# Optimization experiments

Measured on AMD Instinct MI355X. Metric: run time of the kernel, lower is better.

## Reference

```python
import jax, jax.numpy as jnp
import numpy as np

REG_DIAG = 0.01   # per-position regularizer added inside the loop in the original
REG_EPS = 1e-05   # global regularizer added after the loop


def setup_inputs() -> dict:
    key = jax.random.key(0)
    B, C, HW = 32, 128, 3136
    embedding = jax.random.normal(key, (B, C, HW), dtype=jnp.float32)
    return {"embedding": embedding}


def reference(embedding):
    # embedding: (B, C, HW)
    B, C, HW = embedding.shape
    mean = jnp.mean(embedding, axis=0)                     # (C, HW)
    centered = embedding - mean[None, :, :]                # (B, C, HW)
    # Per-position sample covariance: cov[i] = X_m^T X_m / (B-1), X_m = (B, C) slice at position i.
    cov = jnp.einsum('bci,bdi->icd', centered, centered) / (B - 1)  # (HW, C, C)
    eye = jnp.eye(C, dtype=embedding.dtype)
    cov = cov + (REG_DIAG + REG_EPS) * eye[None, :, :]
    inv_covariance = jnp.linalg.inv(cov)                   # batched inverse, (HW, C, C)
    return (mean, inv_covariance)
```

## Files before the change

### kernel.cpp

```cpp
#include <hip/hip_runtime.h>

#define HW 3136
#define NB 32
#define NC 128
#define XST 132
#define SST 36
#define LAMV 0.01001f

static __device__ __forceinline__ float2 pka0(float2 c, float2 v, float2 a) {
  float2 d;
  asm("v_pk_fma_f32 %0, %1, %2, %3 op_sel:[0,0,0] op_sel_hi:[0,1,1]"
      : "=v"(d) : "v"(c), "v"(v), "v"(a));
  return d;
}
static __device__ __forceinline__ float2 pka1(float2 c, float2 v, float2 a) {
  float2 d;
  asm("v_pk_fma_f32 %0, %1, %2, %3 op_sel:[1,0,0] op_sel_hi:[1,1,1]"
      : "=v"(d) : "v"(c), "v"(v), "v"(a));
  return d;
}
static __device__ __forceinline__ float2 pke(float2 a, float2 b, float2 c) {
  float2 d;
  asm("v_pk_fma_f32 %0, %1, %2, %3"
      : "=v"(d) : "v"(a), "v"(b), "v"(c));
  return d;
}

__global__ __launch_bounds__(512, 8)
void mvg_kernel(const float* __restrict__ emb, float* __restrict__ out) {
  const int bid = blockIdx.x;
  const int pos = (bid & 7) * 392 + (bid >> 3);
  const int t = threadIdx.x;

  __shared__ __align__(16) float XcB[NB * XST];
  __shared__ __align__(16) float WB[NB * XST];
  __shared__ __align__(16) float SB[32 * SST];
  __shared__ float ms[NC];

  #pragma unroll
  for (int m = 0; m < 8; ++m) {
    const int idx = t + 512 * m;
    const int b = idx >> 7;
    const int c = idx & (NC - 1);
    XcB[b * XST + c] = emb[(size_t)b * (size_t)(NC * HW) + (size_t)c * HW + pos];
  }
  __syncthreads();

  if (t < NC) {
    float s = 0.f;
    #pragma unroll
    for (int b = 0; b < NB; ++b) s += XcB[b * XST + t];
    const float m = s * (1.0f / NB);
    ms[t] = m;
    out[(size_t)t * HW + pos] = m;
  }
  __syncthreads();

  #pragma unroll
  for (int m = 0; m < 8; ++m) {
    const int idx = t + 512 * m;
    const int b = idx >> 7;
    const int c = idx & (NC - 1);
    XcB[b * XST + c] -= ms[c];
  }
  __syncthreads();

  {
    const int i = t >> 4;
    const int j2 = t & 15;
    const float* xi = &XcB[i * XST];
    const float* xa = &XcB[(2 * j2) * XST];
    const float* xb = &XcB[(2 * j2 + 1) * XST];
    float2 accA = make_float2(0.f, 0.f), accB = make_float2(0.f, 0.f);
    #pragma unroll 8
    for (int c = 0; c < NC; c += 4) {
      const float4 vi = *(const float4*)&xi[c];
      const float4 va = *(const float4*)&xa[c];
      const float4 vb = *(const float4*)&xb[c];
      const float2 viL = make_float2(vi.x, vi.y), viH = make_float2(vi.z, vi.w);
      accA = pke(viL, make_float2(va.x, va.y), accA);
      accA = pke(viH, make_float2(va.z, va.w), accA);
      accB = pke(viL, make_float2(vb.x, vb.y), accB);
      accB = pke(viH, make_float2(vb.z, vb.w), accB);
    }
    const float s31 = 1.0f / 31.0f;
    SB[i * SST + 2 * j2]     = (accA.x + accA.y) * s31 + ((i == 2 * j2)     ? LAMV : 0.f);
    SB[i * SST + 2 * j2 + 1] = (accB.x + accB.y) * s31 + ((i == 2 * j2 + 1) ? LAMV : 0.f);
  }
  __syncthreads();

  if (t < 64) {
    const int r = t & 31;
    const int hb = (t >> 5) << 4;
    float m[16];
    #pragma unroll
    for (int j = 0; j < 4; ++j) {
      const float4 v = *(const float4*)&SB[r * SST + hb + 4 * j];
      m[4 * j] = v.x; m[4 * j + 1] = v.y; m[4 * j + 2] = v.z; m[4 * j + 3] = v.w;
    }

    #define SWEEP_K(K) {                                                    \
      float pc = m[(K) & 15] - ((r == (K)) ? 1.0f : 0.0f);                  \
      const float dm1 = __shfl(pc, (((K) >> 4) << 5) + (K), 64);            \
      const float cr  = __shfl(pc, (((K) >> 4) << 5) + r, 64);              \
      const float g = cr * __builtin_amdgcn_rcpf(dm1 + 1.0f);               \
      float hj[16];                                                         \
      _Pragma("unroll")                                                     \
      for (int j = 0; j < 16; ++j)                                          \
        hj[j] = __shfl(pc, (((K) >> 4) << 5) + hb + j, 64);                 \
      _Pragma("unroll")                                                     \
      for (int j = 0; j < 16; ++j) m[j] = fmaf(-g, hj[j], m[j]);            \
    }

    SWEEP_K(0)  SWEEP_K(1)  SWEEP_K(2)  SWEEP_K(3)
    SWEEP_K(4)  SWEEP_K(5)  SWEEP_K(6)  SWEEP_K(7)
    SWEEP_K(8)  SWEEP_K(9)  SWEEP_K(10) SWEEP_K(11)
    SWEEP_K(12) SWEEP_K(13) SWEEP_K(14) SWEEP_K(15)
    SWEEP_K(16) SWEEP_K(17) SWEEP_K(18) SWEEP_K(19)
    SWEEP_K(20) SWEEP_K(21) SWEEP_K(22) SWEEP_K(23)
    SWEEP_K(24) SWEEP_K(25) SWEEP_K(26) SWEEP_K(27)
    SWEEP_K(28) SWEEP_K(29) SWEEP_K(30) SWEEP_K(31)

    #pragma unroll
    for (int j = 0; j < 16; ++j) {
      const int col = hb + j;
      SB[r * SST + col] = (col == r) ? (2.0f - m[j]) : (-m[j]);
    }
  }
  __syncthreads();

  {
    const int s = t >> 4;
    const int C0 = (t & 15) << 3;
    float2 w01 = make_float2(0.f, 0.f), w23 = make_float2(0.f, 0.f);
    float2 w45 = make_float2(0.f, 0.f), w67 = make_float2(0.f, 0.f);
    #pragma unroll 2
    for (int j = 0; j < 32; j += 4) {
      const float4 sv = *(const float4*)&SB[s * SST + j];
      const float2 svL = make_float2(sv.x, sv.y);
      const float2 svH = make_float2(sv.z, sv.w);
      {
        const float* xr = &XcB[(j + 0) * XST + C0];
        const float4 a = *(const float4*)xr;
        const float4 b = *(const float4*)(xr + 4);
        w01 = pka0(svL, make_float2(a.x, a.y), w01);
        w23 = pka0(svL, make_float2(a.z, a.w), w23);
        w45 = pka0(svL, make_float2(b.x, b.y), w45);
        w67 = pka0(svL, make_float2(b.z, b.w), w67);
      }
      {
        const float* xr = &XcB[(j + 1) * XST + C0];
        const float4 a = *(const float4*)xr;
        const float4 b = *(const float4*)(xr + 4);
        w01 = pka1(svL, make_float2(a.x, a.y), w01);
        w23 = pka1(svL, make_float2(a.z, a.w), w23);
        w45 = pka1(svL, make_float2(b.x, b.y), w45);
        w67 = pka1(svL, make_float2(b.z, b.w), w67);
      }
      {
        const float* xr = &XcB[(j + 2) * XST + C0];
        const float4 a = *(const float4*)xr;
        const float4 b = *(const float4*)(xr + 4);
        w01 = pka0(svH, make_float2(a.x, a.y), w01);
        w23 = pka0(svH, make_float2(a.z, a.w), w23);
        w45 = pka0(svH, make_float2(b.x, b.y), w45);
        w67 = pka0(svH, make_float2(b.z, b.w), w67);
      }
      {
        const float* xr = &XcB[(j + 3) * XST + C0];
        const float4 a = *(const float4*)xr;
        const float4 b = *(const float4*)(xr + 4);
        w01 = pka1(svH, make_float2(a.x, a.y), w01);
        w23 = pka1(svH, make_float2(a.z, a.w), w23);
        w45 = pka1(svH, make_float2(b.x, b.y), w45);
        w67 = pka1(svH, make_float2(b.z, b.w), w67);
      }
    }
    *(float4*)&WB[s * XST + C0]     = make_float4(w01.x, w01.y, w23.x, w23.y);
    *(float4*)&WB[s * XST + C0 + 4] = make_float4(w45.x, w45.y, w67.x, w67.y);
  }
  __syncthreads();

  {
    const int rm = t >> 5;
    const int cm = t & 31;
    const int i0 = rm << 3;
    const int c0 = cm << 2;
    float2 aP[8][2];
    #pragma unroll
    for (int r = 0; r < 8; ++r) {
      aP[r][0] = make_float2(0.f, 0.f);
      aP[r][1] = make_float2(0.f, 0.f);
    }
    #pragma unroll 4
    for (int s = 0; s < 32; ++s) {
      const float4 cv0 = *(const float4*)&XcB[s * XST + i0];
      const float4 cv1 = *(const float4*)&XcB[s * XST + i0 + 4];
      const float4 rv  = *(const float4*)&WB[s * XST + c0];
      const float2 rL = make_float2(rv.x, rv.y), rH = make_float2(rv.z, rv.w);
      const float2 c01 = make_float2(cv0.x, cv0.y), c23 = make_float2(cv0.z, cv0.w);
      const float2 c45 = make_float2(cv1.x, cv1.y), c67 = make_float2(cv1.z, cv1.w);
      aP[0][0] = pka0(c01, rL, aP[0][0]); aP[0][1] = pka0(c01, rH, aP[0][1]);
      aP[1][0] = pka1(c01, rL, aP[1][0]); aP[1][1] = pka1(c01, rH, aP[1][1]);
      aP[2][0] = pka0(c23, rL, aP[2][0]); aP[2][1] = pka0(c23, rH, aP[2][1]);
      aP[3][0] = pka1(c23, rL, aP[3][0]); aP[3][1] = pka1(c23, rH, aP[3][1]);
      aP[4][0] = pka0(c45, rL, aP[4][0]); aP[4][1] = pka0(c45, rH, aP[4][1]);
      aP[5][0] = pka1(c45, rL, aP[5][0]); aP[5][1] = pka1(c45, rH, aP[5][1]);
      aP[6][0] = pka0(c67, rL, aP[6][0]); aP[6][1] = pka0(c67, rH, aP[6][1]);
      aP[7][0] = pka1(c67, rL, aP[7][0]); aP[7][1] = pka1(c67, rH, aP[7][1]);
    }
    const float ILAM = 1.0f / LAMV;
    const float IL31 = ILAM / 31.0f;
    float* o = out + (size_t)NC * HW + (size_t)pos * (NC * NC);
    #pragma unroll
    for (int r = 0; r < 8; ++r) {
      const int gr = i0 + r;
      float4 w;
      w.x = fmaf(-IL31, aP[r][0].x, (gr == c0 + 0) ? ILAM : 0.f);
      w.y = fmaf(-IL31, aP[r][0].y, (gr == c0 + 1) ? ILAM : 0.f);
      w.z = fmaf(-IL31, aP[r][1].x, (gr == c0 + 2) ? ILAM : 0.f);
      w.w = fmaf(-IL31, aP[r][1].y, (gr == c0 + 3) ? ILAM : 0.f);
      *(float4*)&o[(size_t)gr * NC + c0] = w;
    }
  }
}

extern "C" void kernel_launch(void* const* d_in, const int* in_sizes, int n_in,
                              void* d_out, int out_size, void* d_ws, size_t ws_size,
                              hipStream_t stream) {
  const float* emb = (const float*)d_in[0];
  float* out = (float*)d_out;
  mvg_kernel<<<HW, 512, 0, stream>>>(emb, out);
}
```

Measured before the change: 155.5 us.

## Exploit symmetry of inverse covariance and permute batch rows for Gram tiling

The final 128x128 inverse is symmetric, so only the upper-triangular 8x8 block tiles (136 blocks split across 272 threads) are computed, and each off-diagonal tile is written twice, once transposed. Batch rows are stored in permuted order (even/odd split) in shared memory so the 32x32 Gram step can use 16x16 threads, each producing a 2x2 register tile with more reuse. The W = S*Xc step likewise gives each thread two output rows. The intent is to roughly halve the FMA work in the last GEMM and cut LDS traffic. The cost is more idle threads, strided transposed global stores that coalesce less well, and extra index maths including a sqrt.

Result: faster. 145.8 us (-6.3%).

```diff
diff --git a/kernel.cpp b/kernel.cpp
--- a/kernel.cpp
+++ b/kernel.cpp
@@ -6,6 +6,7 @@
 #define XST 132
 #define SST 36
 #define LAMV 0.01001f
+#define SIG(r) (((((r) & 1)) << 4) | ((r) >> 1))
 
 static __device__ __forceinline__ float2 pka0(float2 c, float2 v, float2 a) {
   float2 d;
@@ -42,7 +43,7 @@
     const int idx = t + 512 * m;
     const int b = idx >> 7;
     const int c = idx & (NC - 1);
-    XcB[b * XST + c] = emb[(size_t)b * (size_t)(NC * HW) + (size_t)c * HW + pos];
+    XcB[SIG(b) * XST + c] = emb[(size_t)b * (size_t)(NC * HW) + (size_t)c * HW + pos];
   }
   __syncthreads();
 
@@ -65,37 +66,50 @@
   }
   __syncthreads();
 
-  {
-    const int i = t >> 4;
-    const int j2 = t & 15;
-    const float* xi = &XcB[i * XST];
-    const float* xa = &XcB[(2 * j2) * XST];
-    const float* xb = &XcB[(2 * j2 + 1) * XST];
-    float2 accA = make_float2(0.f, 0.f), accB = make_float2(0.f, 0.f);
+  if (t < 256) {
+    const int I = t >> 4;
+    const int J = t & 15;
+    const float* xi0 = &XcB[I * XST];
+    const float* xi1 = &XcB[(16 + I) * XST];
+    const float* xj0 = &XcB[J * XST];
+    const float* xj1 = &XcB[(16 + J) * XST];
+    float2 d00 = make_float2(0.f, 0.f), d01 = make_float2(0.f, 0.f);
+    float2 d10 = make_float2(0.f, 0.f), d11 = make_float2(0.f, 0.f);
     #pragma unroll 8
     for (int c = 0; c < NC; c += 4) {
-      const float4 vi = *(const float4*)&xi[c];
-      const float4 va = *(const float4*)&xa[c];
-      const float4 vb = *(const float4*)&xb[c];
-      const float2 viL = make_float2(vi.x, vi.y), viH = make_float2(vi.z, vi.w);
-      accA = pke(viL, make_float2(va.x, va.y), accA);
-      accA = pke(viH, make_float2(va.z, va.w), accA);
-      accB = pke(viL, make_float2(vb.x, vb.y), accB);
-      accB = pke(viH, make_float2(vb.z, vb.w), accB);
+      const float4 a0 = *(const float4*)&xi0[c];
+      const float4 a1 = *(const float4*)&xi1[c];
+      const float4 b0 = *(const float4*)&xj0[c];
+      const float4 b1 = *(const float4*)&xj1[c];
+      const float2 a0L = make_float2(a0.x, a0.y), a0H = make_float2(a0.z, a0.w);
+      const float2 a1L = make_float2(a1.x, a1.y), a1H = make_float2(a1.z, a1.w);
+      const float2 b0L = make_float2(b0.x, b0.y), b0H = make_float2(b0.z, b0.w);
+      const float2 b1L = make_float2(b1.x, b1.y), b1H = make_float2(b1.z, b1.w);
+      d00 = pke(a0L, b0L, d00); d00 = pke(a0H, b0H, d00);
+      d01 = pke(a0L, b1L, d01); d01 = pke(a0H, b1H, d01);
+      d10 = pke(a1L, b0L, d10); d10 = pke(a1H, b0H, d10);
+      d11 = pke(a1L, b1L, d11); d11 = pke(a1H, b1H, d11);
     }
     const float s31 = 1.0f / 31.0f;
-    SB[i * SST + 2 * j2]     = (accA.x + accA.y) * s31 + ((i == 2 * j2)     ? LAMV : 0.f);
-    SB[i * SST + 2 * j2 + 1] = (accB.x + accB.y) * s31 + ((i == 2 * j2 + 1) ? LAMV : 0.f);
+    const float dg = (I == J) ? LAMV : 0.f;
+    float2 e0, e1;
+    e0.x = (d00.x + d00.y) * s31 + dg;
+    e0.y = (d01.x + d01.y) * s31;
+    e1.x = (d10.x + d10.y) * s31;
+    e1.y = (d11.x + d11.y) * s31 + dg;
+    *(float2*)&SB[I * SST + 2 * J] = e0;
+    *(float2*)&SB[(16 + I) * SST + 2 * J] = e1;
   }
   __syncthreads();
 
   if (t < 64) {
     const int r = t & 31;
     const int hb = (t >> 5) << 4;
+    const int rs = SIG(r);
     float m[16];
     #pragma unroll
     for (int j = 0; j < 4; ++j) {
-      const float4 v = *(const float4*)&SB[r * SST + hb + 4 * j];
+      const float4 v = *(const float4*)&SB[rs * SST + hb + 4 * j];
       m[4 * j] = v.x; m[4 * j + 1] = v.y; m[4 * j + 2] = v.z; m[4 * j + 3] = v.w;
     }
 
@@ -124,68 +138,96 @@
     #pragma unroll
     for (int j = 0; j < 16; ++j) {
       const int col = hb + j;
-      SB[r * SST + col] = (col == r) ? (2.0f - m[j]) : (-m[j]);
-    }
-  }
-  __syncthreads();
-
-  {
-    const int s = t >> 4;
+      SB[rs * SST + col] = (col == r) ? (2.0f - m[j]) : (-m[j]);
+    }
+  }
+  __syncthreads();
+
+  if (t < 256) {
+    const int s2 = t >> 4;
     const int C0 = (t & 15) << 3;
-    float2 w01 = make_float2(0.f, 0.f), w23 = make_float2(0.f, 0.f);
-    float2 w45 = make_float2(0.f, 0.f), w67 = make_float2(0.f, 0.f);
+    float2 w0[4], w1[4];
+    #pragma unroll
+    for (int q = 0; q < 4; ++q) {
+      w0[q] = make_float2(0.f, 0.f);
+      w1[q] = make_float2(0.f, 0.f);
+    }
     #pragma unroll 2
     for (int j = 0; j < 32; j += 4) {
-      const float4 sv = *(const float4*)&SB[s * SST + j];
-      const float2 svL = make_float2(sv.x, sv.y);
-      const float2 svH = make_float2(sv.z, sv.w);
-      {
-        const float* xr = &XcB[(j + 0) * XST + C0];
-        const float4 a = *(const float4*)xr;
-        const float4 b = *(const float4*)(xr + 4);
-        w01 = pka0(svL, make_float2(a.x, a.y), w01);
-        w23 = pka0(svL, make_float2(a.z, a.w), w23);
-        w45 = pka0(svL, make_float2(b.x, b.y), w45);
-        w67 = pka0(svL, make_float2(b.z, b.w), w67);
-      }
-      {
-        const float* xr = &XcB[(j + 1) * XST + C0];
-        const float4 a = *(const float4*)xr;
-        const float4 b = *(const float4*)(xr + 4);
-        w01 = pka1(svL, make_float2(a.x, a.y), w01);
-        w23 = pka1(svL, make_float2(a.z, a.w), w23);
-        w45 = pka1(svL, make_float2(b.x, b.y), w45);
-        w67 = pka1(svL, make_float2(b.z, b.w), w67);
-      }
-      {
-        const float* xr = &XcB[(j + 2) * XST + C0];
-        const float4 a = *(const float4*)xr;
-        const float4 b = *(const float4*)(xr + 4);
-        w01 = pka0(svH, make_float2(a.x, a.y), w01);
-        w23 = pka0(svH, make_float2(a.z, a.w), w23);
-        w45 = pka0(svH, make_float2(b.x, b.y), w45);
-        w67 = pka0(svH, make_float2(b.z, b.w), w67);
-      }
-      {
-        const float* xr = &XcB[(j + 3) * XST + C0];
-        const float4 a = *(const float4*)xr;
-        const float4 b = *(const float4*)(xr + 4);
-        w01 = pka1(svH, make_float2(a.x, a.y), w01);
-        w23 = pka1(svH, make_float2(a.z, a.w), w23);
-        w45 = pka1(svH, make_float2(b.x, b.y), w45);
-        w67 = pka1(svH, make_float2(b.z, b.w), w67);
-      }
-    }
-    *(float4*)&WB[s * XST + C0]     = make_float4(w01.x, w01.y, w23.x, w23.y);
-    *(float4*)&WB[s * XST + C0 + 4] = make_float4(w45.x, w45.y, w67.x, w67.y);
-  }
-  __syncthreads();
-
-  {
-    const int rm = t >> 5;
-    const int cm = t & 31;
-    const int i0 = rm << 3;
-    const int c0 = cm << 2;
+      const float4 sv0 = *(const float4*)&SB[s2 * SST + j];
+      const float4 sv1 = *(const float4*)&SB[(16 + s2) * SST + j];
+      const float2 s0L = make_float2(sv0.x, sv0.y), s0H = make_float2(sv0.z, sv0.w);
+      const float2 s1L = make_float2(sv1.x, sv1.y), s1H = make_float2(sv1.z, sv1.w);
+      const int jh = j >> 1;
+      const float* xr0 = &XcB[jh * XST + C0];
+      const float* xr1 = &XcB[(16 + jh) * XST + C0];
+      const float* xr2 = &XcB[(jh + 1) * XST + C0];
+      const float* xr3 = &XcB[(16 + jh + 1) * XST + C0];
+      {
+        const float4 a = *(const float4*)xr0;
+        const float4 b = *(const float4*)(xr0 + 4);
+        w0[0] = pka0(s0L, make_float2(a.x, a.y), w0[0]);
+        w0[1] = pka0(s0L, make_float2(a.z, a.w), w0[1]);
+        w0[2] = pka0(s0L, make_float2(b.x, b.y), w0[2]);
+        w0[3] = pka0(s0L, make_float2(b.z, b.w), w0[3]);
+        w1[0] = pka0(s1L, make_float2(a.x, a.y), w1[0]);
+        w1[1] = pka0(s1L, make_float2(a.z, a.w), w1[1]);
+        w1[2] = pka0(s1L, make_float2(b.x, b.y), w1[2]);
+        w1[3] = pka0(s1L, make_float2(b.z, b.w), w1[3]);
+      }
+      {
+        const float4 a = *(const float4*)xr1;
+        const float4 b = *(const float4*)(xr1 + 4);
+        w0[0] = pka1(s0L, make_float2(a.x, a.y), w0[0]);
+        w0[1] = pka1(s0L, make_float2(a.z, a.w), w0[1]);
+        w0[2] = pka1(s0L, make_float2(b.x, b.y), w0[2]);
+        w0[3] = pka1(s0L, make_float2(b.z, b.w), w0[3]);
+        w1[0] = pka1(s1L, make_float2(a.x, a.y), w1[0]);
+        w1[1] = pka1(s1L, make_float2(a.z, a.w), w1[1]);
+        w1[2] = pka1(s1L, make_float2(b.x, b.y), w1[2]);
+        w1[3] = pka1(s1L, make_float2(b.z, b.w), w1[3]);
+      }
+      {
+        const float4 a = *(const float4*)xr2;
+        const float4 b = *(const float4*)(xr2 + 4);
+        w0[0] = pka0(s0H, make_float2(a.x, a.y), w0[0]);
+        w0[1] = pka0(s0H, make_float2(a.z, a.w), w0[1]);
+        w0[2] = pka0(s0H, make_float2(b.x, b.y), w0[2]);
+        w0[3] = pka0(s0H, make_float2(b.z, b.w), w0[3]);
+        w1[0] = pka0(s1H, make_float2(a.x, a.y), w1[0]);
+        w1[1] = pka0(s1H, make_float2(a.z, a.w), w1[1]);
+        w1[2] = pka0(s1H, make_float2(b.x, b.y), w1[2]);
+        w1[3] = pka0(s1H, make_float2(b.z, b.w), w1[3]);
+      }
+      {
+        const float4 a = *(const float4*)xr3;
+        const float4 b = *(const float4*)(xr3 + 4);
+        w0[0] = pka1(s0H, make_float2(a.x, a.y), w0[0]);
+        w0[1] = pka1(s0H, make_float2(a.z, a.w), w0[1]);
+        w0[2] = pka1(s0H, make_float2(b.x, b.y), w0[2]);
+        w0[3] = pka1(s0H, make_float2(b.z, b.w), w0[3]);
+        w1[0] = pka1(s1H, make_float2(a.x, a.y), w1[0]);
+        w1[1] = pka1(s1H, make_float2(a.z, a.w), w1[1]);
+        w1[2] = pka1(s1H, make_float2(b.x, b.y), w1[2]);
+        w1[3] = pka1(s1H, make_float2(b.z, b.w), w1[3]);
+      }
+    }
+    *(float4*)&WB[s2 * XST + C0]     = make_float4(w0[0].x, w0[0].y, w0[1].x, w0[1].y);
+    *(float4*)&WB[s2 * XST + C0 + 4] = make_float4(w0[2].x, w0[2].y, w0[3].x, w0[3].y);
+    *(float4*)&WB[(16 + s2) * XST + C0]     = make_float4(w1[0].x, w1[0].y, w1[1].x, w1[1].y);
+    *(float4*)&WB[(16 + s2) * XST + C0 + 4] = make_float4(w1[2].x, w1[2].y, w1[3].x, w1[3].y);
+  }
+  __syncthreads();
+
+  if (t < 272) {
+    const int L = t >> 1;
+    const int half = t & 1;
+    const float fs = sqrtf(1089.0f - 8.0f * (float)L);
+    const int R = (int)floorf((33.0f - fs) * 0.5f);
+    const int C = R + L - (R * (33 - R)) / 2;
+    const int r8 = R << 3;
+    const int cb = (C << 3) + (half << 2);
+
     float2 aP[8][2];
     #pragma unroll
     for (int r = 0; r < 8; ++r) {
@@ -193,10 +235,10 @@
       aP[r][1] = make_float2(0.f, 0.f);
     }
     #pragma unroll 4
-    for (int s = 0; s < 32; ++s) {
-      const float4 cv0 = *(const float4*)&XcB[s * XST + i0];
-      const float4 cv1 = *(const float4*)&XcB[s * XST + i0 + 4];
-      const float4 rv  = *(const float4*)&WB[s * XST + c0];
+    for (int u = 0; u < 32; ++u) {
+      const float4 cv0 = *(const float4*)&XcB[u * XST + r8];
+      const float4 cv1 = *(const float4*)&XcB[u * XST + r8 + 4];
+      const float4 rv  = *(const float4*)&WB[u * XST + cb];
       const float2 rL = make_float2(rv.x, rv.y), rH = make_float2(rv.z, rv.w);
       const float2 c01 = make_float2(cv0.x, cv0.y), c23 = make_float2(cv0.z, cv0.w);
       const float2 c45 = make_float2(cv1.x, cv1.y), c67 = make_float2(cv1.z, cv1.w);
@@ -209,18 +251,55 @@
       aP[6][0] = pka0(c67, rL, aP[6][0]); aP[6][1] = pka0(c67, rH, aP[6][1]);
       aP[7][0] = pka1(c67, rL, aP[7][0]); aP[7][1] = pka1(c67, rH, aP[7][1]);
     }
+
     const float ILAM = 1.0f / LAMV;
     const float IL31 = ILAM / 31.0f;
     float* o = out + (size_t)NC * HW + (size_t)pos * (NC * NC);
+
     #pragma unroll
     for (int r = 0; r < 8; ++r) {
-      const int gr = i0 + r;
+      const int gr = r8 + r;
       float4 w;
-      w.x = fmaf(-IL31, aP[r][0].x, (gr == c0 + 0) ? ILAM : 0.f);
-      w.y = fmaf(-IL31, aP[r][0].y, (gr == c0 + 1) ? ILAM : 0.f);
-      w.z = fmaf(-IL31, aP[r][1].x, (gr == c0 + 2) ? ILAM : 0.f);
-      w.w = fmaf(-IL31, aP[r][1].y, (gr == c0 + 3) ? ILAM : 0.f);
-      *(float4*)&o[(size_t)gr * NC + c0] = w;
+      w.x = fmaf(-IL31, aP[r][0].x, (gr == cb + 0) ? ILAM : 0.f);
+      w.y = fmaf(-IL31, aP[r][0].y, (gr == cb + 1) ? ILAM : 0.f);
+      w.z = fmaf(-IL31, aP[r][1].x, (gr == cb + 2) ? ILAM : 0.f);
+      w.w = fmaf(-IL31, aP[r][1].y, (gr == cb + 3) ? ILAM : 0.f);
+      *(float4*)&o[(size_t)gr * NC + cb] = w;
+    }
+
+    if (R != C) {
+      {
+        const float4 m0 = make_float4(-IL31 * aP[0][0].x, -IL31 * aP[1][0].x,
+                                      -IL31 * aP[2][0].x, -IL31 * aP[3][0].x);
+        const float4 m1 = make_float4(-IL31 * aP[4][0].x, -IL31 * aP[5][0].x,
+                                      -IL31 * aP[6][0].x, -IL31 * aP[7][0].x);
+        *(float4*)&o[(size_t)(cb + 0) * NC + r8] = m0;
+        *(float4*)&o[(size_t)(cb + 0) * NC + r8 + 4] = m1;
+      }
+      {
+        const float4 m0 = make_float4(-IL31 * aP[0][0].y, -IL31 * aP[1][0].y,
+                                      -IL31 * aP[2][0].y, -IL31 * aP[3][0].y);
+        const float4 m1 = make_float4(-IL31 * aP[4][0].y, -IL31 * aP[5][0].y,
+                                      -IL31 * aP[6][0].y, -IL31 * aP[7][0].y);
+        *(float4*)&o[(size_t)(cb + 1) * NC + r8] = m0;
+        *(float4*)&o[(size_t)(cb + 1) * NC + r8 + 4] = m1;
+      }
+      {
+        const float4 m0 = make_float4(-IL31 * aP[0][1].x, -IL31 * aP[1][1].x,
+                                      -IL31 * aP[2][1].x, -IL31 * aP[3][1].x);
+        const float4 m1 = make_float4(-IL31 * aP[4][1].x, -IL31 * aP[5][1].x,
+                                      -IL31 * aP[6][1].x, -IL31 * aP[7][1].x);
+        *(float4*)&o[(size_t)(cb + 2) * NC + r8] = m0;
+        *(float4*)&o[(size_t)(cb + 2) * NC + r8 + 4] = m1;
+      }
+      {
+        const float4 m0 = make_float4(-IL31 * aP[0][1].y, -IL31 * aP[1][1].y,
+                                      -IL31 * aP[2][1].y, -IL31 * aP[3][1].y);
+        const float4 m1 = make_float4(-IL31 * aP[4][1].y, -IL31 * aP[5][1].y,
+                                      -IL31 * aP[6][1].y, -IL31 * aP[7][1].y);
+        *(float4*)&o[(size_t)(cb + 3) * NC + r8] = m0;
+        *(float4*)&o[(size_t)(cb + 3) * NC + r8 + 4] = m1;
+      }
     }
   }
 }
```
